# Performance work log

Measured on AMD Instinct MI355X. Metric: run time of the kernel, lower is better.

The kernel has to match this reference:

```python
import jax, jax.numpy as jnp
import numpy as np
import math

D_MODEL = 1024
NUM_HEADS = 16
D_K = D_MODEL // NUM_HEADS
THETA = 10000.0
NEG_INF = 1.0e6  # module uses -1e6, not -inf


def _rope_tables(seq_len):
    pair_idx = jnp.arange(0, D_K, 2, dtype=jnp.float32)
    inv_freq = 1.0 / (THETA ** (pair_idx / D_K))
    pos = jnp.arange(seq_len, dtype=jnp.float32)
    angles = jnp.outer(pos, inv_freq)  # (S, D_K//2)
    return jnp.cos(angles), jnp.sin(angles)


def _apply_rope(x, cos, sin):
    # x: (B, H, S, D_K); cos/sin: (S, D_K//2)
    xe = x[..., 0::2]
    xo = x[..., 1::2]
    oe = xe * cos - xo * sin
    oo = xe * sin + xo * cos
    return jnp.stack([oe, oo], axis=-1).reshape(x.shape)


def setup_inputs() -> dict:
    key = jax.random.key(0)
    k0, k1, k2, k3, k4 = jax.random.split(key, 5)
    B, S = 2, 2048
    x = jax.random.normal(k0, (B, S, D_MODEL), dtype=jnp.float32)
    scale = 0.02
    wq = jax.random.normal(k1, (D_MODEL, D_MODEL), dtype=jnp.float32) * scale
    wk = jax.random.normal(k2, (D_MODEL, D_MODEL), dtype=jnp.float32) * scale
    wv = jax.random.normal(k3, (D_MODEL, D_MODEL), dtype=jnp.float32) * scale
    wo = jax.random.normal(k4, (D_MODEL, D_MODEL), dtype=jnp.float32) * scale
    return {"x": x, "wq": wq, "wk": wk, "wv": wv, "wo": wo}


def reference(x, wq, wk, wv, wo):
    B, S, _ = x.shape
    q = x @ wq.T
    k = x @ wk.T
    v = x @ wv.T
    # (B, S, H, d_k) -> (B, H, S, d_k)
    q = q.reshape(B, S, NUM_HEADS, D_K).transpose(0, 2, 1, 3)
    k = k.reshape(B, S, NUM_HEADS, D_K).transpose(0, 2, 1, 3)
    v = v.reshape(B, S, NUM_HEADS, D_K).transpose(0, 2, 1, 3)
    cos, sin = _rope_tables(S)
    q = _apply_rope(q, cos, sin)
    k = _apply_rope(k, cos, sin)
    scores = jnp.einsum("bhqd,bhkd->bhqk", q, k) / math.sqrt(D_K)
    causal = jnp.tril(jnp.ones((S, S), dtype=bool))
    scores = jnp.where(causal, scores, -NEG_INF)
    attn = jax.nn.softmax(scores, axis=-1)
    out = jnp.einsum("bhqk,bhkd->bhqd", attn, v)
    out = out.transpose(0, 2, 1, 3).reshape(B, S, D_MODEL)
    return out @ wo.T
```

## Files before the change

kernel.cpp:

```cpp
#include <hip/hip_runtime.h>

typedef __attribute__((ext_vector_type(8))) __bf16 bf16x8;
typedef __attribute__((ext_vector_type(8))) _Float16 f16x8;
typedef __attribute__((ext_vector_type(4))) float f32x4;
typedef __attribute__((ext_vector_type(8))) unsigned short u16x8;
typedef __attribute__((ext_vector_type(4))) unsigned int u32x4;

#define MFMA_BF16(a, b, c) __builtin_amdgcn_mfma_f32_16x16x32_bf16((a), (b), (c), 0, 0, 0)
#define MFMA_F16(a, b, c)  __builtin_amdgcn_mfma_f32_16x16x32_f16((a), (b), (c), 0, 0, 0)
#define LOG2E 1.44269504088896340736f
#define QSCALE 0.18033688011112042f

__device__ __forceinline__ float b2f(unsigned short u) {
    union { unsigned int i; float f; } v; v.i = ((unsigned int)u) << 16; return v.f;
}
__device__ __forceinline__ unsigned short f2bf(float f) {
    union { float f; unsigned int i; } v; v.f = f;
    unsigned int u = v.i;
    return (unsigned short)((u + 0x7fffu + ((u >> 16) & 1u)) >> 16);
}

__device__ __forceinline__ void gl_lds16(const void* g, void* l) {
    __builtin_amdgcn_global_load_lds(
        (const __attribute__((address_space(1))) void*)g,
        (__attribute__((address_space(3))) void*)l,
        16, 0, 0);
}

__global__ __launch_bounds__(256) void cvt_all(const float* __restrict__ x,
                                               const float* __restrict__ wq,
                                               const float* __restrict__ wk,
                                               const float* __restrict__ wv,
                                               const float* __restrict__ wo,
                                               unsigned short* __restrict__ xb,
                                               unsigned short* __restrict__ wqb,
                                               unsigned short* __restrict__ wkb,
                                               unsigned short* __restrict__ wvb,
                                               unsigned short* __restrict__ wob) {
    int id = blockIdx.x * 256 + threadIdx.x;
    const float* src; unsigned short* dst; size_t off; float scl = 1.0f;
    if (id < 524288)      { src = x;  dst = xb;  off = (size_t)id * 8; }
    else if (id < 655360) { src = wq; dst = wqb; off = (size_t)(id - 524288) * 8; scl = QSCALE; }
    else if (id < 786432) { src = wk; dst = wkb; off = (size_t)(id - 655360) * 8; }
    else if (id < 917504) { src = wv; dst = wvb; off = (size_t)(id - 786432) * 8; }
    else                  { src = wo; dst = wob; off = (size_t)(id - 917504) * 8; }
    float4 a = *(const float4*)(src + off);
    float4 b = *(const float4*)(src + off + 4);
    u16x8 o;
    o[0] = f2bf(a.x * scl); o[1] = f2bf(a.y * scl); o[2] = f2bf(a.z * scl); o[3] = f2bf(a.w * scl);
    o[4] = f2bf(b.x * scl); o[5] = f2bf(b.y * scl); o[6] = f2bf(b.z * scl); o[7] = f2bf(b.w * scl);
    *(u16x8*)(dst + off) = o;
}

template <int MODE>
__device__ __forceinline__ void gemm128_bt(const unsigned short* __restrict__ A,
                                           const unsigned short* __restrict__ B,
                                           void* __restrict__ Cv,
                                           int m0, int n0, int ldc,
                                           unsigned short* As, unsigned short* Bs) {
    const int tid = threadIdx.x;
    const int w = tid >> 6, lane = tid & 63;
    const int quad = lane >> 4, l15 = lane & 15;
    const int wm = w & 1, wn = w >> 1;

    f32x4 acc[4][4];
#pragma unroll
    for (int mt = 0; mt < 4; ++mt)
#pragma unroll
        for (int nt = 0; nt < 4; ++nt) acc[mt][nt] = f32x4{0.f, 0.f, 0.f, 0.f};

    for (int k0 = 0; k0 < 1024; k0 += 32) {
        __syncthreads();
#pragma unroll
        for (int i = 0; i < 2; ++i) {
            int L = (w * 2 + i) * 64 + lane;
            int r = L >> 2;
            int c = (L & 3) ^ ((r >> 1) & 3);
            gl_lds16(A + (size_t)(m0 + r) * 1024 + k0 + c * 8, As + L * 8);
            gl_lds16(B + (size_t)(n0 + r) * 1024 + k0 + c * 8, Bs + L * 8);
        }
        __syncthreads();

        bf16x8 af[4], bfr[4];
#pragma unroll
        for (int mt = 0; mt < 4; ++mt) {
            int row = wm * 64 + mt * 16 + l15;
            af[mt] = *(const bf16x8*)(As + row * 32 + (quad ^ ((row >> 1) & 3)) * 8);
        }
#pragma unroll
        for (int nt = 0; nt < 4; ++nt) {
            int row = wn * 64 + nt * 16 + l15;
            bfr[nt] = *(const bf16x8*)(Bs + row * 32 + (quad ^ ((row >> 1) & 3)) * 8);
        }
#pragma unroll
        for (int mt = 0; mt < 4; ++mt)
#pragma unroll
            for (int nt = 0; nt < 4; ++nt)
                acc[mt][nt] = MFMA_BF16(af[mt], bfr[nt], acc[mt][nt]);
    }

    float invf[4], sgn = 0.f;
    if constexpr (MODE == 3) {
        sgn = (l15 & 1) ? 1.0f : -1.0f;
#pragma unroll
        for (int nt = 0; nt < 4; ++nt)
            invf[nt] = exp2f(-0.41524101186092029f * (float)((nt * 16 + l15) >> 1));
    }

#pragma unroll
    for (int mt = 0; mt < 4; ++mt) {
        int grow = m0 + wm * 64 + mt * 16 + quad * 4;
#pragma unroll
        for (int nt = 0; nt < 4; ++nt) {
            int gcol = n0 + wn * 64 + nt * 16 + l15;
#pragma unroll
            for (int r = 0; r < 4; ++r) {
                float val = acc[mt][nt][r];
                size_t idx = (size_t)(grow + r) * ldc + gcol;
                if constexpr (MODE == 0) {
                    ((unsigned short*)Cv)[idx] = f2bf(val);
                } else if constexpr (MODE == 1) {
                    ((float*)Cv)[idx] = val;
                } else if constexpr (MODE == 2) {
                    _Float16 hv = (_Float16)val;
                    ((unsigned short*)Cv)[idx] = __builtin_bit_cast(unsigned short, hv);
                } else {
                    float p = __shfl_xor(val, 1);
                    float pos = (float)((grow + r) & 2047);
                    float ang = pos * invf[nt];
                    float out = val * __cosf(ang) + sgn * p * __sinf(ang);
                    ((unsigned short*)Cv)[idx] = f2bf(out);
                }
            }
        }
    }
}

__global__ __launch_bounds__(256) void gemm_qkv(const unsigned short* __restrict__ X,
                                                const unsigned short* __restrict__ Wq,
                                                const unsigned short* __restrict__ Wk,
                                                const unsigned short* __restrict__ Wv,
                                                unsigned short* __restrict__ Qo,
                                                unsigned short* __restrict__ Ko,
                                                unsigned short* __restrict__ Vt) {
    __shared__ unsigned short As[128 * 32];
    __shared__ unsigned short Bs[128 * 32];
    int y = blockIdx.y;
    if (y < 16) {
        int sel = y >> 3;
        int m0 = blockIdx.x * 128;
        int n0 = (y & 7) * 128;
        const unsigned short* B = sel ? Wk : Wq;
        unsigned short* C = sel ? Ko : Qo;
        gemm128_bt<3>(X, B, C, m0, n0, 1024, As, Bs);
    } else {
        int m0 = (y & 7) * 128;
        int n0 = blockIdx.x * 128;
        gemm128_bt<2>(Wv, X, Vt, m0, n0, 4096, As, Bs);
    }
}

__global__ __launch_bounds__(256) void gemm_out(const unsigned short* __restrict__ A,
                                                const unsigned short* __restrict__ Wo,
                                                float* __restrict__ C) {
    __shared__ unsigned short As[128 * 32];
    __shared__ unsigned short Bs[128 * 32];
    gemm128_bt<1>(A, Wo, C, blockIdx.x * 128, blockIdx.y * 128, 1024, As, Bs);
}

#define FBODY(KBASE, MASKED)                                                            \
    {                                                                                   \
        bf16x8 kf[4][2];                                                                \
        _Pragma("unroll")                                                               \
        for (int nt = 0; nt < 4; ++nt) {                                                \
            int row = nt * 16 + l15;                                                    \
            const unsigned short* kp = Ksb + row * 64;                                  \
            int swk = row & 7;                                                          \
            kf[nt][0] = *(const bf16x8*)(kp + (quad ^ swk) * 8);                        \
            kf[nt][1] = *(const bf16x8*)(kp + ((quad ^ 4) ^ swk) * 8);                  \
        }                                                                               \
        f16x8 pa[2][2];                                                                 \
        _Pragma("unroll")                                                               \
        for (int mt = 0; mt < 2; ++mt) {                                                \
            f32x4 sc[4];                                                                \
            _Pragma("unroll")                                                           \
            for (int nt = 0; nt < 4; ++nt) {                                            \
                f32x4 z = f32x4{0.f, 0.f, 0.f, 0.f};                                    \
                z = MFMA_BF16(kf[nt][0], qf[mt][0], z);                                 \
                sc[nt] = MFMA_BF16(kf[nt][1], qf[mt][1], z);                            \
            }                                                                           \
            int qpos = qposw + mt * 16 + l15;                                           \
            unsigned pk[8];                                                             \
            _Pragma("unroll")                                                           \
            for (int nt = 0; nt < 4; ++nt) {                                            \
                float e[4];                                                             \
                _Pragma("unroll")                                                       \
                for (int r_ = 0; r_ < 4; ++r_) {                                        \
                    float ev = exp2f(sc[nt][r_]);                                       \
                    if (MASKED) {                                                       \
                        int kpos = (KBASE) + nt * 16 + quad * 4 + r_;                   \
                        ev = (kpos > qpos) ? 0.f : ev;                                  \
                    }                                                                   \
                    e[r_] = ev;                                                         \
                }                                                                       \
                pk[nt * 2 + 0] = __builtin_bit_cast(unsigned,                           \
                                     __builtin_amdgcn_cvt_pkrtz(e[0], e[1]));           \
                pk[nt * 2 + 1] = __builtin_bit_cast(unsigned,                           \
                                     __builtin_amdgcn_cvt_pkrtz(e[2], e[3]));           \
            }                                                                           \
            u32x4 rs0 = u32x4{pk[0], pk[1], pk[2], pk[3]};                              \
            u32x4 rs1 = u32x4{pk[4], pk[5], pk[6], pk[7]};                              \
            lacc[mt] = MFMA_F16(__builtin_bit_cast(f16x8, rs0), ones, lacc[mt]);        \
            lacc[mt] = MFMA_F16(__builtin_bit_cast(f16x8, rs1), ones, lacc[mt]);        \
            int b0 = quad & 1;                                                          \
            unsigned y0 = (unsigned)__builtin_amdgcn_ds_swizzle(                        \
                              (int)(b0 ? pk[0] : pk[2]), 0x401F);                       \
            unsigned y1 = (unsigned)__builtin_amdgcn_ds_swizzle(                        \
                              (int)(b0 ? pk[1] : pk[3]), 0x401F);                       \
            unsigned y2 = (unsigned)__builtin_amdgcn_ds_swizzle(                        \
                              (int)(b0 ? pk[4] : pk[6]), 0x401F);                       \
            unsigned y3 = (unsigned)__builtin_amdgcn_ds_swizzle(                        \
                              (int)(b0 ? pk[5] : pk[7]), 0x401F);                       \
            u32x4 t0 = b0 ? u32x4{y0, y1, pk[2], pk[3]}                                 \
                          : u32x4{pk[0], pk[1], y0, y1};                                \
            u32x4 t1 = b0 ? u32x4{y2, y3, pk[6], pk[7]}                                 \
                          : u32x4{pk[4], pk[5], y2, y3};                                \
            pa[mt][0] = __builtin_bit_cast(f16x8, t0);                                  \
            pa[mt][1] = __builtin_bit_cast(f16x8, t1);                                  \
        }                                                                               \
        _Pragma("unroll")                                                               \
        for (int nt = 0; nt < 4; ++nt) {                                                \
            int rowd = nt * 16 + l15;                                                   \
            const unsigned short* vp = Vsb + rowd * 64;                                 \
            int sl0 = pi4 ^ (rowd & 7);                                                 \
            f16x8 v0 = *(const f16x8*)(vp + sl0 * 8);                                   \
            f16x8 v1 = *(const f16x8*)(vp + (sl0 ^ 4) * 8);                             \
            accO[0][nt] = MFMA_F16(pa[0][0], v0, accO[0][nt]);                          \
            accO[1][nt] = MFMA_F16(pa[1][0], v0, accO[1][nt]);                          \
            accO[0][nt] = MFMA_F16(pa[0][1], v1, accO[0][nt]);                          \
            accO[1][nt] = MFMA_F16(pa[1][1], v1, accO[1][nt]);                          \
        }                                                                               \
    }

__global__ __launch_bounds__(512, 4) void flash_attn(const unsigned short* __restrict__ Q,
                                                     const unsigned short* __restrict__ Kb,
                                                     const unsigned short* __restrict__ Vt,
                                                     unsigned short* __restrict__ O) {
    int id = blockIdx.x;
    int xcd = id & 7;
    int s  = id >> 3;
    int rr = s & 3;
    int t  = s >> 2;
    int qt = (t < 8) ? t : 23 - t;
    int bh = xcd + 8 * rr;
    int b = bh >> 4, h = bh & 15;
    int tid = threadIdx.x;
    int wv8 = tid >> 6;
    int g = wv8 >> 2;
    int w = wv8 & 3;
    int lane = tid & 63;
    int quad = lane >> 4, l15 = lane & 15;
    int pi4 = ((quad & 1) << 1) | (quad >> 1);

    __shared__ __align__(16) float Red[10240];
    unsigned short* Ks = (unsigned short*)Red;
    unsigned short* Vs = Ks + 8192;

    int r = tid >> 3, c = (tid & 7) ^ (r & 7);
    const unsigned short* KgT = Kb + (size_t)(b * 2048 + r) * 1024 + h * 64 + c * 8;
    const unsigned short* VgT = Vt + (size_t)(h * 64 + r) * 4096 + b * 2048 + c * 8;

    int qrow0 = b * 2048 + qt * 128 + w * 32;
    int qposw = qt * 128 + w * 32;
    int nit = qt + 1;

    bf16x8 qf[2][2];
#pragma unroll
    for (int mt = 0; mt < 2; ++mt) {
        const unsigned short* qp =
            Q + (size_t)(qrow0 + mt * 16 + l15) * 1024 + h * 64 + quad * 8;
        qf[mt][0] = *(const bf16x8*)qp;
        qf[mt][1] = *(const bf16x8*)(qp + 32);
    }

    f16x8 ones;
#pragma unroll
    for (int tt = 0; tt < 8; ++tt) ones[tt] = (_Float16)1.0f;

    f32x4 accO[2][4];
    f32x4 lacc[2];
#pragma unroll
    for (int mt = 0; mt < 2; ++mt) {
        lacc[mt] = f32x4{0.f, 0.f, 0.f, 0.f};
#pragma unroll
        for (int nt = 0; nt < 4; ++nt) accO[mt][nt] = f32x4{0.f, 0.f, 0.f, 0.f};
    }

    for (int it = 0; it < nit; ++it) {
        __syncthreads();
        {
            size_t ko = (size_t)(it * 128) * 1024;
            int vo = it * 128;
            gl_lds16(KgT + ko, Ks + tid * 8);
            gl_lds16(KgT + ko + 64 * 1024, Ks + 4096 + tid * 8);
            gl_lds16(VgT + vo, Vs + tid * 8);
            gl_lds16(VgT + vo + 64, Vs + 4096 + tid * 8);
        }
        __syncthreads();
        const unsigned short* Ksb = Ks + g * 4096;
        const unsigned short* Vsb = Vs + g * 4096;
        int kbase = it * 128 + g * 64;
        if (it < nit - 1) {
            FBODY(kbase, 0)
        } else {
            FBODY(kbase, 1)
        }
    }

    __syncthreads();
    if (g == 1) {
        float* dst = Red + (size_t)(w * 64 + lane) * 4;
#pragma unroll
        for (int mt = 0; mt < 2; ++mt)
#pragma unroll
            for (int nt = 0; nt < 4; ++nt)
                *(f32x4*)(dst + (mt * 4 + nt) * 1024) = accO[mt][nt];
        *(f32x4*)(dst + 8 * 1024) = lacc[0];
        *(f32x4*)(dst + 9 * 1024) = lacc[1];
    }
    __syncthreads();
    if (g == 0) {
        const float* src = Red + (size_t)(w * 64 + lane) * 4;
#pragma unroll
        for (int mt = 0; mt < 2; ++mt)
#pragma unroll
            for (int nt = 0; nt < 4; ++nt)
                accO[mt][nt] += *(const f32x4*)(src + (mt * 4 + nt) * 1024);
        lacc[0] += *(const f32x4*)(src + 8 * 1024);
        lacc[1] += *(const f32x4*)(src + 9 * 1024);

#pragma unroll
        for (int mt = 0; mt < 2; ++mt) {
            float inv[4];
#pragma unroll
            for (int r_ = 0; r_ < 4; ++r_) inv[r_] = 1.0f / lacc[mt][r_];
#pragma unroll
            for (int nt = 0; nt < 4; ++nt)
#pragma unroll
                for (int r_ = 0; r_ < 4; ++r_)
                    O[(size_t)(qrow0 + mt * 16 + quad * 4 + r_) * 1024 +
                      h * 64 + nt * 16 + l15] = f2bf(accO[mt][nt][r_] * inv[r_]);
        }
    }
}

extern "C" void kernel_launch(void* const* d_in, const int* in_sizes, int n_in,
                              void* d_out, int out_size, void* d_ws, size_t ws_size,
                              hipStream_t stream) {
    (void)in_sizes; (void)n_in; (void)out_size; (void)ws_size;
    const float* x  = (const float*)d_in[0];
    const float* wq = (const float*)d_in[1];
    const float* wk = (const float*)d_in[2];
    const float* wv = (const float*)d_in[3];
    const float* wo = (const float*)d_in[4];
    float* out = (float*)d_out;

    const size_t T = (size_t)4096 * 1024;
    const size_t W = (size_t)1024 * 1024;
    unsigned short* Q   = (unsigned short*)d_ws;
    unsigned short* K   = Q + T;
    unsigned short* Vt  = K + T;
    unsigned short* xb  = Vt + T;
    unsigned short* AO  = xb;
    unsigned short* wqb = xb + T;
    unsigned short* wkb = wqb + W;
    unsigned short* wvb = wkb + W;
    unsigned short* wob = wvb + W;

    cvt_all  <<<dim3(4096),   256, 0, stream>>>(x, wq, wk, wv, wo, xb, wqb, wkb, wvb, wob);
    gemm_qkv <<<dim3(32, 24), 256, 0, stream>>>(xb, wqb, wkb, wvb, Q, K, Vt);
    flash_attn<<<dim3(512),   512, 0, stream>>>(Q, K, Vt, AO);
    gemm_out <<<dim3(32, 8),  256, 0, stream>>>(AO, wob, out);
}
```

Before: 178.9 us.

## Double-buffer LDS tiles in projection GEMMs to overlap global loads with MFMA

```diff
diff --git a/kernel.cpp b/kernel.cpp
--- a/kernel.cpp
+++ b/kernel.cpp
@@ -52,6 +52,20 @@
     *(u16x8*)(dst + off) = o;
 }
 
+#define GSTAGE(k0_, buf_)                                                   \
+    {                                                                       \
+        _Pragma("unroll")                                                   \
+        for (int i = 0; i < 2; ++i) {                                       \
+            int L = (w * 2 + i) * 64 + lane;                                \
+            int r = L >> 2;                                                 \
+            int c = (L & 3) ^ ((r >> 1) & 3);                               \
+            gl_lds16(A + (size_t)(m0 + r) * 1024 + (k0_) + c * 8,           \
+                     As + (buf_) * 4096 + L * 8);                           \
+            gl_lds16(B + (size_t)(n0 + r) * 1024 + (k0_) + c * 8,           \
+                     Bs + (buf_) * 4096 + L * 8);                           \
+        }                                                                   \
+    }
+
 template <int MODE>
 __device__ __forceinline__ void gemm128_bt(const unsigned short* __restrict__ A,
                                            const unsigned short* __restrict__ B,
@@ -69,34 +83,36 @@
 #pragma unroll
         for (int nt = 0; nt < 4; ++nt) acc[mt][nt] = f32x4{0.f, 0.f, 0.f, 0.f};
 
+    GSTAGE(0, 0)
+    __asm__ volatile("s_waitcnt vmcnt(0)" ::: "memory");
+    __builtin_amdgcn_s_barrier();
+
+    int buf = 0;
     for (int k0 = 0; k0 < 1024; k0 += 32) {
-        __syncthreads();
-#pragma unroll
-        for (int i = 0; i < 2; ++i) {
-            int L = (w * 2 + i) * 64 + lane;
-            int r = L >> 2;
-            int c = (L & 3) ^ ((r >> 1) & 3);
-            gl_lds16(A + (size_t)(m0 + r) * 1024 + k0 + c * 8, As + L * 8);
-            gl_lds16(B + (size_t)(n0 + r) * 1024 + k0 + c * 8, Bs + L * 8);
-        }
-        __syncthreads();
-
+        if (k0 + 32 < 1024) GSTAGE(k0 + 32, buf ^ 1)
+
+        const unsigned short* Asb = As + buf * 4096;
+        const unsigned short* Bsb = Bs + buf * 4096;
         bf16x8 af[4], bfr[4];
 #pragma unroll
         for (int mt = 0; mt < 4; ++mt) {
             int row = wm * 64 + mt * 16 + l15;
-            af[mt] = *(const bf16x8*)(As + row * 32 + (quad ^ ((row >> 1) & 3)) * 8);
+            af[mt] = *(const bf16x8*)(Asb + row * 32 + (quad ^ ((row >> 1) & 3)) * 8);
         }
 #pragma unroll
         for (int nt = 0; nt < 4; ++nt) {
             int row = wn * 64 + nt * 16 + l15;
-            bfr[nt] = *(const bf16x8*)(Bs + row * 32 + (quad ^ ((row >> 1) & 3)) * 8);
+            bfr[nt] = *(const bf16x8*)(Bsb + row * 32 + (quad ^ ((row >> 1) & 3)) * 8);
         }
 #pragma unroll
         for (int mt = 0; mt < 4; ++mt)
 #pragma unroll
             for (int nt = 0; nt < 4; ++nt)
                 acc[mt][nt] = MFMA_BF16(af[mt], bfr[nt], acc[mt][nt]);
+
+        __asm__ volatile("s_waitcnt vmcnt(0) lgkmcnt(0)" ::: "memory");
+        __builtin_amdgcn_s_barrier();
+        buf ^= 1;
     }
 
     float invf[4], sgn = 0.f;
@@ -135,6 +151,7 @@
         }
     }
 }
+#undef GSTAGE
 
 __global__ __launch_bounds__(256) void gemm_qkv(const unsigned short* __restrict__ X,
                                                 const unsigned short* __restrict__ Wq,
@@ -143,8 +160,8 @@
                                                 unsigned short* __restrict__ Qo,
                                                 unsigned short* __restrict__ Ko,
                                                 unsigned short* __restrict__ Vt) {
-    __shared__ unsigned short As[128 * 32];
-    __shared__ unsigned short Bs[128 * 32];
+    __shared__ unsigned short As[2 * 128 * 32];
+    __shared__ unsigned short Bs[2 * 128 * 32];
     int y = blockIdx.y;
     if (y < 16) {
         int sel = y >> 3;
@@ -163,8 +180,8 @@
 __global__ __launch_bounds__(256) void gemm_out(const unsigned short* __restrict__ A,
                                                 const unsigned short* __restrict__ Wo,
                                                 float* __restrict__ C) {
-    __shared__ unsigned short As[128 * 32];
-    __shared__ unsigned short Bs[128 * 32];
+    __shared__ unsigned short As[2 * 128 * 32];
+    __shared__ unsigned short Bs[2 * 128 * 32];
     gemm128_bt<1>(A, Wo, C, blockIdx.x * 128, blockIdx.y * 128, 1024, As, Bs);
 }
 
```

After: 195.5 us. 9.3% more time.
